# Kernel tuning notes

Hardware: AMD Instinct MI355X
Metric: run time of the kernel (lower is better)

The kernel has to match this reference:

```python
import jax, jax.numpy as jnp
import numpy as np

N, E, D, H = 50000, 800000, 128, 4
DH = D // H
BN_EPS = 1e-5


def setup_inputs() -> dict:
    key = jax.random.key(0)
    ks = jax.random.split(key, 16)
    s = 0.02
    inp = {
        "x": jax.random.normal(ks[0], (N, D), dtype=jnp.float32),
        "edge_index": jax.random.randint(ks[1], (2, E), 0, N, dtype=jnp.int64),
        "Wk": jax.random.normal(ks[2], (D, D), dtype=jnp.float32) * s,
        "bk": jnp.zeros((D,), jnp.float32),
        "Wm": jax.random.normal(ks[3], (D, D), dtype=jnp.float32) * s,
        "bm": jnp.zeros((D,), jnp.float32),
        "Wq": jax.random.normal(ks[4], (D, D), dtype=jnp.float32) * s,
        "bq": jnp.zeros((D,), jnp.float32),
        "W1": jax.random.normal(ks[5], (D, D), dtype=jnp.float32) * s,
        "b1": jnp.zeros((D,), jnp.float32),
        "gamma": jnp.ones((D,), jnp.float32),
        "beta": jnp.zeros((D,), jnp.float32),
        "W2": jax.random.normal(ks[6], (D, D), dtype=jnp.float32) * s,
        "b2": jnp.zeros((D,), jnp.float32),
    }
    return inp


def reference(x, edge_index, Wk, bk, Wm, bm, Wq, bq, W1, b1, gamma, beta, W2, b2):
    src = edge_index[0]  # [E] softmax segment key
    dst = edge_index[1]  # [E] aggregation target
    x_i = x[dst]         # [E, D] (torch code: X[1])
    x_j = x[src]         # [E, D] (torch code: X[0])

    key = (x_i @ Wk + bk).reshape(-1, H, DH)
    msg = (x_j @ Wm + bm).reshape(-1, H, DH)
    query = (x_j @ Wq + bq).reshape(-1, H, DH) / jnp.sqrt(jnp.float32(DH))

    scores = jnp.sum(query * key, axis=2)  # [E, H]

    # segment softmax over src node index (numerically stable)
    smax = jax.ops.segment_max(scores, src, num_segments=N)
    e = jnp.exp(scores - smax[src])
    ssum = jax.ops.segment_sum(e, src, num_segments=N)
    alpha = e / ssum[src]  # [E, H]

    # rescale by per-src-node edge count
    cnt = jax.ops.segment_sum(jnp.ones((scores.shape[0],), jnp.float32), src, num_segments=N)
    alpha = alpha * cnt[src][:, None]

    out_e = (msg * alpha[:, :, None]).reshape(-1, D)  # [E, D]
    out = jax.ops.segment_sum(out_e, dst, num_segments=N)  # [N, D]

    # MLP: Linear -> BatchNorm1d (training-mode batch stats) -> ReLU -> Linear
    h = out @ W1 + b1
    mean = jnp.mean(h, axis=0)
    var = jnp.var(h, axis=0)  # biased variance, as torch BN uses for normalization
    h = (h - mean) * jax.lax.rsqrt(var + BN_EPS) * gamma + beta
    h = jax.nn.relu(h)
    return h @ W2 + b2
```

## Files before the change

kernel.cpp:

```cpp
#include <hip/hip_runtime.h>
#include <hip/hip_bf16.h>

#define N_NODES 50000
#define N_EDGES 800000
#define DIM 128
#define NHEAD 4
#define GEMM_BLOCKS 782
#define HBLOCKS 313
#define EPB 2560
#define NBUCK 196
#define NBUCK2 392
#define NODE_PAD 50432
#define N2 (2 * N_NODES)

typedef __bf16 bf16x8 __attribute__((ext_vector_type(8)));
typedef __bf16 bf16x2 __attribute__((ext_vector_type(2)));
typedef float f32x4 __attribute__((ext_vector_type(4)));

struct WPtrs { const float* w[5]; };

__global__ __launch_bounds__(256) void prep_weights(WPtrs P, __bf16* __restrict__ Wt)
{
  __shared__ __bf16 tileT[16][136];
  const int mat = blockIdx.x >> 3, sl = blockIdx.x & 7;
  const float* W = P.w[mat];
  const int col0 = sl * 16;
  const int t = threadIdx.x;
  #pragma unroll
  for (int i = 0; i < 8; ++i) {
    int id = t + i * 256;
    int k = id >> 4, c = id & 15;
    tileT[c][k] = (__bf16)W[k * 128 + col0 + c];
  }
  __syncthreads();
  int c = t >> 4, kb = t & 15;
  bf16x8 v = *(const bf16x8*)&tileT[c][kb * 8];
  *(bf16x8*)&Wt[(size_t)mat * 16384 + (size_t)(col0 + c) * 128 + kb * 8] = v;
}


__device__ __forceinline__ void stage_Wt_half(const __bf16* __restrict__ Wt,
    int half, __bf16 (*wLDS)[136])
{
  const int t = threadIdx.x;
  const __bf16* base = Wt + (size_t)half * 64 * 128;
  #pragma unroll
  for (int i = 0; i < 4; ++i) {
    int id = t + i * 256;
    int col = id >> 4, kb = id & 15;
    bf16x8 v = ((const bf16x8*)(base + (size_t)col * 128))[kb];
    *(bf16x8*)&wLDS[col][kb * 8] = v;
  }
}

__device__ __forceinline__ void stage_A_f32(const float* __restrict__ A, int row0,
    int nrows, __bf16 (*aLDS)[136])
{
  const int t = threadIdx.x;
  #pragma unroll
  for (int i = 0; i < 4; ++i) {
    int id = t + i * 256;
    int r = id >> 4, cb = id & 15;
    int gr = row0 + r;
    float4 v0 = make_float4(0.f, 0.f, 0.f, 0.f), v1 = v0;
    if (gr < nrows) {
      const float4* row = (const float4*)(A + (size_t)gr * DIM);
      v0 = row[cb * 2];
      v1 = row[cb * 2 + 1];
    }
    bf16x8 o;
    o[0] = (__bf16)v0.x; o[1] = (__bf16)v0.y; o[2] = (__bf16)v0.z; o[3] = (__bf16)v0.w;
    o[4] = (__bf16)v1.x; o[5] = (__bf16)v1.y; o[6] = (__bf16)v1.z; o[7] = (__bf16)v1.w;
    *(bf16x8*)&aLDS[r][cb * 8] = o;
  }
}

__device__ __forceinline__ void stage_A_bf16(const __bf16* __restrict__ A, int row0,
    int nrows, __bf16 (*aLDS)[136])
{
  const int t = threadIdx.x;
  #pragma unroll
  for (int i = 0; i < 4; ++i) {
    int id = t + i * 256;
    int r = id >> 4, cb = id & 15;
    int gr = row0 + r;
    bf16x8 v = {};
    if (gr < nrows) v = ((const bf16x8*)(A + (size_t)gr * DIM))[cb];
    *(bf16x8*)&aLDS[r][cb * 8] = v;
  }
}

__device__ __forceinline__ void mfma_half(const __bf16 (*aLDS)[136],
    const __bf16 (*wLDS)[136], int half, f32x4 acc[8])
{
  const int lane = threadIdx.x & 63, wave = threadIdx.x >> 6;
  const int m = lane & 15, q = lane >> 4;
  #pragma unroll
  for (int kt = 0; kt < 4; ++kt) {
    bf16x8 a = *(const bf16x8*)&aLDS[wave * 16 + m][kt * 32 + q * 8];
    #pragma unroll
    for (int ct = 0; ct < 4; ++ct) {
      bf16x8 b = *(const bf16x8*)&wLDS[ct * 16 + m][kt * 32 + q * 8];
      acc[half * 4 + ct] =
          __builtin_amdgcn_mfma_f32_16x16x32_bf16(a, b, acc[half * 4 + ct], 0, 0, 0);
    }
  }
}

template <typename OutT>
__device__ __forceinline__ void store_tile(f32x4 acc[8],
    const float* __restrict__ bias, float scale, OutT* __restrict__ C,
    int row0, int nrows)
{
  const int lane = threadIdx.x & 63, wave = threadIdx.x >> 6;
  const int m = lane & 15, q = lane >> 4;
  #pragma unroll
  for (int j = 0; j < 8; ++j) {
    int col = (j >> 2) * 64 + (j & 3) * 16 + m;
    float bv = bias[col];
    #pragma unroll
    for (int r = 0; r < 4; ++r) {
      int row = row0 + wave * 16 + q * 4 + r;
      if (row < nrows) C[(size_t)row * DIM + col] = (OutT)((acc[j][r] + bv) * scale);
    }
  }
}

__device__ __forceinline__ void gemm_pass(const __bf16 (*aLDS)[136],
    __bf16 (*wLDS)[136], const __bf16* __restrict__ Wt, f32x4 acc[8])
{
  #pragma unroll
  for (int i = 0; i < 8; ++i) acc[i] = (f32x4){0.f, 0.f, 0.f, 0.f};
  stage_Wt_half(Wt, 0, wLDS);
  __syncthreads();
  mfma_half(aLDS, wLDS, 0, acc);
  __syncthreads();
  stage_Wt_half(Wt, 1, wLDS);
  __syncthreads();
  mfma_half(aLDS, wLDS, 1, acc);
}

__global__ __launch_bounds__(256) void fat1(const int* __restrict__ ei,
    int* __restrict__ hist,
    const __bf16* __restrict__ Wt, const float* __restrict__ x,
    const float* __restrict__ bk, const float* __restrict__ bm,
    const float* __restrict__ bq,
    __bf16* __restrict__ Kn, __bf16* __restrict__ Mn, __bf16* __restrict__ Qn)
{
  __shared__ __bf16 aLDS[64][136];
  __shared__ __bf16 wLDS[64][136];
  const int b = blockIdx.x, t = threadIdx.x;

  if (b < HBLOCKS) {
    int* h = (int*)&aLDS[0][0];
    for (int i = t; i < NBUCK2; i += 256) h[i] = 0;
    __syncthreads();
    #pragma unroll
    for (int i = 0; i < 10; ++i) {
      int e = b * EPB + i * 256 + t;
      if (e < N_EDGES) {
        int s = ei[e], d = ei[N_EDGES + e];
        atomicAdd(&h[s >> 8], 1);
        atomicAdd(&h[NBUCK + (d >> 8)], 1);
      }
    }
    __syncthreads();
    for (int i = t; i < NBUCK2; i += 256) hist[b * NBUCK2 + i] = h[i];
  } else {
    const int row0 = (b - HBLOCKS) * 64;
    f32x4 acc[8];
    stage_A_f32(x, row0, N_NODES, aLDS);
    gemm_pass(aLDS, wLDS, Wt, acc);
    store_tile<__bf16>(acc, bk, 1.0f, Kn, row0, N_NODES);
    __syncthreads();
    gemm_pass(aLDS, wLDS, Wt + 16384, acc);
    store_tile<__bf16>(acc, bm, 1.0f, Mn, row0, N_NODES);
    __syncthreads();
    gemm_pass(aLDS, wLDS, Wt + 32768, acc);
    store_tile<__bf16>(acc, bq, 0.17677669529663689f, Qn, row0, N_NODES);
  }
}

__global__ __launch_bounds__(64) void bucket_scan(const int* __restrict__ hist,
    int* __restrict__ bbase, int* __restrict__ tot)
{
  const int b = blockIdx.x, l = threadIdx.x;
  int run = 0;
  for (int c = 0; c < 5; ++c) {
    int idx = c * 64 + l;
    int v = (idx < HBLOCKS) ? hist[idx * NBUCK2 + b] : 0;
    int orig = v;
    #pragma unroll
    for (int o = 1; o < 64; o <<= 1) {
      int n = __shfl_up(v, o);
      if (l >= o) v += n;
    }
    if (idx < HBLOCKS) bbase[idx * NBUCK2 + b] = run + v - orig;
    run += __shfl(v, 63);
  }
  if (l == 0) tot[b] = run;
}

__global__ __launch_bounds__(256) void bucket_starts(const int* __restrict__ tot,
    int* __restrict__ bstart)
{
  __shared__ int s[256];
  const int t = threadIdx.x;
  int v = (t < NBUCK) ? tot[t] : 0;
  s[t] = v; __syncthreads();
  for (int o = 1; o < 256; o <<= 1) {
    int x = (t >= o) ? s[t - o] : 0; __syncthreads();
    s[t] += x; __syncthreads();
  }
  if (t < NBUCK) bstart[t] = s[t] - v;
  __syncthreads();
  v = (t < NBUCK) ? tot[NBUCK + t] : 0;
  s[t] = v; __syncthreads();
  for (int o = 1; o < 256; o <<= 1) {
    int x = (t >= o) ? s[t - o] : 0; __syncthreads();
    s[t] += x; __syncthreads();
  }
  if (t < NBUCK) bstart[NBUCK + t] = s[t] - v;
}

__global__ __launch_bounds__(256) void edge_scatter(const int* __restrict__ ei,
    const int* __restrict__ bbase, const int* __restrict__ bstart,
    int2* __restrict__ bucketedS, int2* __restrict__ bucketedD)
{
  __shared__ int base[NBUCK2];
  __shared__ int cur[NBUCK2];
  const int b = blockIdx.x, t = threadIdx.x;
  for (int i = t; i < NBUCK2; i += 256) {
    base[i] = bstart[i] + bbase[b * NBUCK2 + i];
    cur[i] = 0;
  }
  __syncthreads();
  #pragma unroll
  for (int i = 0; i < 10; ++i) {
    int e = b * EPB + i * 256 + t;
    if (e < N_EDGES) {
      int s = ei[e], d = ei[N_EDGES + e];
      int pk = s | (d << 16);
      int bs = s >> 8, bd = NBUCK + (d >> 8);
      int lo = atomicAdd(&cur[bs], 1);
      bucketedS[base[bs] + lo] = make_int2(pk, e);
      int ld = atomicAdd(&cur[bd], 1);
      bucketedD[base[bd] + ld] = make_int2(pk, e);
    }
  }
}

__global__ __launch_bounds__(256) void bucket_rank(const int2* __restrict__ bucketedS,
    const int2* __restrict__ bucketedD, const int* __restrict__ bstart,
    const int* __restrict__ tot,
    int2* __restrict__ elistS, int2* __restrict__ elistD,
    int* __restrict__ starts, int* __restrict__ deg,
    int* __restrict__ startsD, int* __restrict__ degD)
{
  __shared__ int c1[256], ns[256], c2[256];
  const int b = blockIdx.x, t = threadIdx.x;
  const bool srcSide = (b < NBUCK);
  const int bb = srcSide ? b : b - NBUCK;
  const int seg0 = bstart[b];
  const int cnt = tot[b];
  const int2* ent = (srcSide ? bucketedS : bucketedD) + seg0;

  c1[t] = 0; c2[t] = 0;
  __syncthreads();
  for (int i = t; i < cnt; i += 256) {
    unsigned pk = (unsigned)ent[i].x;
    int ln = (int)(srcSide ? (pk & 0xFFFFu) : (pk >> 16)) - (bb << 8);
    atomicAdd(&c1[ln], 1);
  }
  __syncthreads();
  ns[t] = c1[t]; __syncthreads();
  for (int o = 1; o < 256; o <<= 1) {
    int x = (t >= o) ? ns[t - o] : 0; __syncthreads();
    ns[t] += x; __syncthreads();
  }
  {
    int node = (bb << 8) + t;
    int nst = ns[t] - c1[t];
    if (srcSide) { starts[node] = seg0 + nst; deg[node] = c1[t]; }
    else         { startsD[node] = seg0 + nst; degD[node] = c1[t]; }
  }
  __syncthreads();
  ns[t] -= c1[t];
  __syncthreads();
  for (int i = t; i < cnt; i += 256) {
    int2 en = ent[i];
    unsigned pk = (unsigned)en.x;
    int ln = (int)(srcSide ? (pk & 0xFFFFu) : (pk >> 16)) - (bb << 8);
    int r = atomicAdd(&c2[ln], 1);
    int pos = seg0 + ns[ln] + r;
    int other = (int)(srcSide ? (pk >> 16) : (pk & 0xFFFFu));
    if (srcSide) elistS[pos] = make_int2(other, en.y);
    else         elistD[pos] = make_int2(other, en.y);
  }
}

__global__ __launch_bounds__(256) void src_scores(const int* __restrict__ starts,
    const int* __restrict__ degS, const int2* __restrict__ elistS,
    const __bf16* __restrict__ Qn, const __bf16* __restrict__ Kn,
    __bf16* __restrict__ Mn, float* __restrict__ wexp)
{
  const int wave = threadIdx.x >> 6, l = threadIdx.x & 63;
  const int n = blockIdx.x * 4 + wave;
  const int g = l >> 4, il = l & 15;
  const int h = il >> 2;
  const int beg = starts[n], end = beg + degS[n];
  if (beg == end) return;

  bf16x8 q8 = ((const bf16x8*)(Qn + (size_t)n * DIM))[il];
  float wsum = 0.f;

  for (int p0 = beg; p0 < end; p0 += 16) {
    int pp[4]; int2 en[4];
    #pragma unroll
    for (int u = 0; u < 4; ++u) {
      pp[u] = p0 + u * 4 + g;
      en[u] = elistS[min(pp[u], end - 1)];
    }
    bf16x8 kk[4];
    #pragma unroll
    for (int u = 0; u < 4; ++u)
      kk[u] = ((const bf16x8*)(Kn + (size_t)en[u].x * DIM))[il];
    #pragma unroll
    for (int u = 0; u < 4; ++u) {
      float pr = 0.f;
      #pragma unroll
      for (int j = 0; j < 8; ++j) pr += (float)q8[j] * (float)kk[u][j];
      pr += __shfl_xor(pr, 1);
      pr += __shfl_xor(pr, 2);
      float w = (pp[u] < end) ? __expf(pr) : 0.f;
      wsum += w;
      if ((pp[u] < end) && (il & 3) == 0) wexp[(size_t)en[u].y * NHEAD + h] = w;
    }
  }
  wsum += __shfl_xor(wsum, 16);
  wsum += __shfl_xor(wsum, 32);
  float factor = (float)(end - beg) / wsum;

  float fm = __shfl(factor, (l >> 4) << 2);
  bf16x2* mrow = (bf16x2*)(Mn + (size_t)n * DIM);
  bf16x2 mv = mrow[l];
  mv[0] = (__bf16)((float)mv[0] * fm);
  mv[1] = (__bf16)((float)mv[1] * fm);
  mrow[l] = mv;
}

__global__ __launch_bounds__(256) void dst_aggregate(const int* __restrict__ startsD,
    const int* __restrict__ degD, const int2* __restrict__ elistD,
    const __bf16* __restrict__ Mn, const float* __restrict__ wexp,
    __bf16* __restrict__ agg)
{
  const int wave = threadIdx.x >> 6, l = threadIdx.x & 63;
  const int n = blockIdx.x * 4 + wave;
  const int g = l >> 4, il = l & 15;
  const int h = il >> 2;
  const int beg = startsD[n], end = beg + degD[n];

  float acc[8];
  #pragma unroll
  for (int j = 0; j < 8; ++j) acc[j] = 0.f;

  for (int q0 = beg; q0 < end; q0 += 16) {
    int qq[4]; int2 ss[4];
    #pragma unroll
    for (int u = 0; u < 4; ++u) {
      qq[u] = q0 + u * 4 + g;
      ss[u] = elistD[min(qq[u], end - 1)];
    }
    float aa[4];
    #pragma unroll
    for (int u = 0; u < 4; ++u) aa[u] = wexp[(size_t)ss[u].y * NHEAD + h];
    bf16x8 mm[4];
    #pragma unroll
    for (int u = 0; u < 4; ++u)
      mm[u] = ((const bf16x8*)(Mn + (size_t)ss[u].x * DIM))[il];
    #pragma unroll
    for (int u = 0; u < 4; ++u) {
      float av = (qq[u] < end) ? aa[u] : 0.f;
      #pragma unroll
      for (int j = 0; j < 8; ++j) acc[j] += (float)mm[u][j] * av;
    }
  }
  #pragma unroll
  for (int j = 0; j < 8; ++j) {
    acc[j] += __shfl_xor(acc[j], 16);
    acc[j] += __shfl_xor(acc[j], 32);
  }
  if (g == 0) {
    bf16x8 o;
    #pragma unroll
    for (int j = 0; j < 8; ++j) o[j] = (__bf16)acc[j];
    *(bf16x8*)(agg + (size_t)n * DIM + il * 8) = o;
  }
}

__global__ __launch_bounds__(256) void gemm_stats(const __bf16* __restrict__ A,
    const __bf16* __restrict__ Wt, const float* __restrict__ bias,
    __bf16* __restrict__ C, float* __restrict__ colsum, float* __restrict__ colsq)
{
  __shared__ __bf16 aLDS[64][136];
  __shared__ __bf16 wLDS[64][136];
  __shared__ float csum[128], csq[128];
  const int t = threadIdx.x;
  const int row0 = blockIdx.x * 64;

  stage_A_bf16(A, row0, N_NODES, aLDS);
  if (t < 128) { csum[t] = 0.f; csq[t] = 0.f; }
  f32x4 acc[8];
  gemm_pass(aLDS, wLDS, Wt, acc);

  const int lane = t & 63, wave = t >> 6;
  const int m = lane & 15, q = lane >> 4;
  #pragma unroll
  for (int j = 0; j < 8; ++j) {
    int col = (j >> 2) * 64 + (j & 3) * 16 + m;
    float bv = bias[col];
    float s = 0.f, s2 = 0.f;
    #pragma unroll
    for (int r = 0; r < 4; ++r) {
      int row = row0 + wave * 16 + q * 4 + r;
      float hv = acc[j][r] + bv;
      if (row < N_NODES) {
        C[(size_t)row * DIM + col] = (__bf16)hv;
        s += hv; s2 += hv * hv;
      }
    }
    s  += __shfl_xor(s, 16);  s  += __shfl_xor(s, 32);
    s2 += __shfl_xor(s2, 16); s2 += __shfl_xor(s2, 32);
    if (q == 0) {
      atomicAdd(&csum[col], s);
      atomicAdd(&csq[col], s2);
    }
  }
  __syncthreads();
  if (t < 128) {
    atomicAdd(&colsum[t], csum[t]);
    atomicAdd(&colsq[t], csq[t]);
  }
}

__global__ __launch_bounds__(256) void gemm_bn(const __bf16* __restrict__ A,
    const __bf16* __restrict__ Wt, const float* __restrict__ bias,
    float* __restrict__ C, const float* __restrict__ colsum,
    const float* __restrict__ colsq, const float* __restrict__ gamma,
    const float* __restrict__ beta)
{
  __shared__ __bf16 aLDS[64][136];
  __shared__ __bf16 wLDS[64][136];
  __shared__ float sA[128], sB[128];
  const int t = threadIdx.x;
  const int row0 = blockIdx.x * 64;

  if (t < 128) {
    float mean = colsum[t] * (1.0f / N_NODES);
    float var = colsq[t] * (1.0f / N_NODES) - mean * mean;
    float inv = rsqrtf(var + 1e-5f);
    float a = gamma[t] * inv;
    sA[t] = a;
    sB[t] = beta[t] - mean * a;
  }
  __syncthreads();

  {
    const int cb = t & 15;
    float sa[8], sb[8];
    #pragma unroll
    for (int j = 0; j < 8; ++j) { sa[j] = sA[cb * 8 + j]; sb[j] = sB[cb * 8 + j]; }
    #pragma unroll
    for (int i = 0; i < 4; ++i) {
      int id = t + i * 256;
      int r = id >> 4;
      int gr = row0 + r;
      bf16x8 v = {};
      if (gr < N_NODES) v = ((const bf16x8*)(A + (size_t)gr * DIM))[cb];
      bf16x8 o;
      #pragma unroll
      for (int j = 0; j < 8; ++j)
        o[j] = (__bf16)fmaxf((float)v[j] * sa[j] + sb[j], 0.f);
      *(bf16x8*)&aLDS[r][cb * 8] = o;
    }
  }
  f32x4 acc[8];
  gemm_pass(aLDS, wLDS, Wt, acc);
  store_tile<float>(acc, bias, 1.0f, C, row0, N_NODES);
}

extern "C" void kernel_launch(void* const* d_in, const int* in_sizes, int n_in,
                              void* d_out, int out_size, void* d_ws, size_t ws_size,
                              hipStream_t stream) {
  const float* x     = (const float*)d_in[0];
  const int*   ei    = (const int*)d_in[1];
  const float* Wk    = (const float*)d_in[2];
  const float* bk    = (const float*)d_in[3];
  const float* Wm    = (const float*)d_in[4];
  const float* bm    = (const float*)d_in[5];
  const float* Wq    = (const float*)d_in[6];
  const float* bq    = (const float*)d_in[7];
  const float* W1    = (const float*)d_in[8];
  const float* b1    = (const float*)d_in[9];
  const float* gamma = (const float*)d_in[10];
  const float* beta  = (const float*)d_in[11];
  const float* W2    = (const float*)d_in[12];
  const float* b2    = (const float*)d_in[13];

  float* ws = (float*)d_ws;
  const size_t ND  = (size_t)N_NODES * DIM;
  const size_t NDh = ND / 2;
  const size_t EH  = (size_t)N_EDGES * NHEAD;

  __bf16* Kn   = (__bf16*)ws;
  __bf16* Mn   = (__bf16*)(ws + NDh);
  __bf16* Qn   = (__bf16*)(ws + 2 * NDh);
  __bf16* agg  = (__bf16*)(ws + 3 * NDh);
  __bf16* h1   = (__bf16*)(ws + 4 * NDh);
  float*  wexp = ws + 5 * NDh;
  int2*   bucketedS = (int2*)wexp;
  int2*   bucketedD = bucketedS + N_EDGES;
  int2*   elistS = (int2*)(wexp + EH);
  int2*   elistD = elistS + N_EDGES;
  int*    hist   = (int*)(elistD + N_EDGES);
  int*    bbase  = hist + HBLOCKS * NBUCK2;
  int*    tot    = bbase + HBLOCKS * NBUCK2;
  int*    bstart = tot + NBUCK2;
  int*    starts = bstart + NBUCK2;
  int*    deg    = starts + NODE_PAD;
  int*    startsD= deg + NODE_PAD;
  int*    degD   = startsD + NODE_PAD;
  float*  colsum = (float*)(degD + NODE_PAD);
  float*  colsq  = colsum + 128;
  __bf16* Wt     = (__bf16*)(colsq + 128);
  float*  outp   = (float*)d_out;

  hipMemsetAsync(colsum, 0, 256 * sizeof(float), stream);

  const int node_blocks = N_NODES / 4;

  WPtrs wp; wp.w[0] = Wk; wp.w[1] = Wm; wp.w[2] = Wq; wp.w[3] = W1; wp.w[4] = W2;
  prep_weights<<<40, 256, 0, stream>>>(wp, Wt);

  fat1<<<HBLOCKS + GEMM_BLOCKS, 256, 0, stream>>>(
      ei, hist, Wt, x, bk, bm, bq, Kn, Mn, Qn);

  bucket_scan<<<NBUCK2, 64, 0, stream>>>(hist, bbase, tot);
  bucket_starts<<<1, 256, 0, stream>>>(tot, bstart);
  edge_scatter<<<HBLOCKS, 256, 0, stream>>>(ei, bbase, bstart, bucketedS, bucketedD);
  bucket_rank<<<NBUCK2, 256, 0, stream>>>(bucketedS, bucketedD, bstart, tot,
                                          elistS, elistD, starts, deg,
                                          startsD, degD);

  src_scores<<<node_blocks, 256, 0, stream>>>(starts, deg, elistS, Qn, Kn, Mn, wexp);
  dst_aggregate<<<node_blocks, 256, 0, stream>>>(startsD, degD, elistD, Mn, wexp, agg);

  gemm_stats<<<GEMM_BLOCKS, 256, 0, stream>>>(agg, Wt + 3 * 16384, b1, h1,
                                              colsum, colsq);
  gemm_bn<<<GEMM_BLOCKS, 256, 0, stream>>>(h1, Wt + 4 * 16384, b2, outp,
                                           colsum, colsq, gamma, beta);
}
```

Measured before the change: 292.1 us.

## Store edge weights in dst order and stage the full weight matrix once

The bucket-rank pass is split into a dst pass, which records each edge's position in the dst-sorted list, and a src pass that carries that position. src_scores can then write edge weights directly in dst order, so dst_aggregate reads them contiguously instead of gathering by edge id. The per-src normalization factor now goes into a small per-node array instead of being applied in place to Mn, and dst_aggregate multiplies it in. The GEMMs also stage the whole 128x128 weight tile in LDS at once, replacing two halves with extra barriers, which doubles LDS use per block and may lower occupancy.

```diff
diff --git a/kernel.cpp b/kernel.cpp
--- a/kernel.cpp
+++ b/kernel.cpp
@@ -11,10 +11,8 @@
 #define NBUCK 196
 #define NBUCK2 392
 #define NODE_PAD 50432
-#define N2 (2 * N_NODES)
 
 typedef __bf16 bf16x8 __attribute__((ext_vector_type(8)));
-typedef __bf16 bf16x2 __attribute__((ext_vector_type(2)));
 typedef float f32x4 __attribute__((ext_vector_type(4)));
 
 struct WPtrs { const float* w[5]; };
@@ -39,16 +37,15 @@
 }
 
 
-__device__ __forceinline__ void stage_Wt_half(const __bf16* __restrict__ Wt,
-    int half, __bf16 (*wLDS)[136])
-{
-  const int t = threadIdx.x;
-  const __bf16* base = Wt + (size_t)half * 64 * 128;
-  #pragma unroll
-  for (int i = 0; i < 4; ++i) {
+__device__ __forceinline__ void stage_Wt_full(const __bf16* __restrict__ Wt,
+    __bf16 (*wLDS)[136])
+{
+  const int t = threadIdx.x;
+  #pragma unroll
+  for (int i = 0; i < 8; ++i) {
     int id = t + i * 256;
     int col = id >> 4, kb = id & 15;
-    bf16x8 v = ((const bf16x8*)(base + (size_t)col * 128))[kb];
+    bf16x8 v = ((const bf16x8*)(Wt + (size_t)col * 128))[kb];
     *(bf16x8*)&wLDS[col][kb * 8] = v;
   }
 }
@@ -90,21 +87,25 @@
   }
 }
 
-__device__ __forceinline__ void mfma_half(const __bf16 (*aLDS)[136],
-    const __bf16 (*wLDS)[136], int half, f32x4 acc[8])
-{
+__device__ __forceinline__ void gemm_full(const __bf16 (*aLDS)[136],
+    __bf16 (*wLDS)[136], const __bf16* __restrict__ Wt, f32x4 acc[8])
+{
+  #pragma unroll
+  for (int i = 0; i < 8; ++i) acc[i] = (f32x4){0.f, 0.f, 0.f, 0.f};
+  stage_Wt_full(Wt, wLDS);
+  __syncthreads();
   const int lane = threadIdx.x & 63, wave = threadIdx.x >> 6;
   const int m = lane & 15, q = lane >> 4;
   #pragma unroll
   for (int kt = 0; kt < 4; ++kt) {
     bf16x8 a = *(const bf16x8*)&aLDS[wave * 16 + m][kt * 32 + q * 8];
     #pragma unroll
-    for (int ct = 0; ct < 4; ++ct) {
+    for (int ct = 0; ct < 8; ++ct) {
       bf16x8 b = *(const bf16x8*)&wLDS[ct * 16 + m][kt * 32 + q * 8];
-      acc[half * 4 + ct] =
-          __builtin_amdgcn_mfma_f32_16x16x32_bf16(a, b, acc[half * 4 + ct], 0, 0, 0);
-    }
-  }
+      acc[ct] = __builtin_amdgcn_mfma_f32_16x16x32_bf16(a, b, acc[ct], 0, 0, 0);
+    }
+  }
+  __syncthreads();
 }
 
 template <typename OutT>
@@ -116,7 +117,7 @@
   const int m = lane & 15, q = lane >> 4;
   #pragma unroll
   for (int j = 0; j < 8; ++j) {
-    int col = (j >> 2) * 64 + (j & 3) * 16 + m;
+    int col = j * 16 + m;
     float bv = bias[col];
     #pragma unroll
     for (int r = 0; r < 4; ++r) {
@@ -124,20 +125,6 @@
       if (row < nrows) C[(size_t)row * DIM + col] = (OutT)((acc[j][r] + bv) * scale);
     }
   }
-}
-
-__device__ __forceinline__ void gemm_pass(const __bf16 (*aLDS)[136],
-    __bf16 (*wLDS)[136], const __bf16* __restrict__ Wt, f32x4 acc[8])
-{
-  #pragma unroll
-  for (int i = 0; i < 8; ++i) acc[i] = (f32x4){0.f, 0.f, 0.f, 0.f};
-  stage_Wt_half(Wt, 0, wLDS);
-  __syncthreads();
-  mfma_half(aLDS, wLDS, 0, acc);
-  __syncthreads();
-  stage_Wt_half(Wt, 1, wLDS);
-  __syncthreads();
-  mfma_half(aLDS, wLDS, 1, acc);
 }
 
 __global__ __launch_bounds__(256) void fat1(const int* __restrict__ ei,
@@ -148,7 +135,7 @@
     __bf16* __restrict__ Kn, __bf16* __restrict__ Mn, __bf16* __restrict__ Qn)
 {
   __shared__ __bf16 aLDS[64][136];
-  __shared__ __bf16 wLDS[64][136];
+  __shared__ __bf16 wLDS[128][136];
   const int b = blockIdx.x, t = threadIdx.x;
 
   if (b < HBLOCKS) {
@@ -170,13 +157,11 @@
     const int row0 = (b - HBLOCKS) * 64;
     f32x4 acc[8];
     stage_A_f32(x, row0, N_NODES, aLDS);
-    gemm_pass(aLDS, wLDS, Wt, acc);
+    gemm_full(aLDS, wLDS, Wt, acc);
     store_tile<__bf16>(acc, bk, 1.0f, Kn, row0, N_NODES);
-    __syncthreads();
-    gemm_pass(aLDS, wLDS, Wt + 16384, acc);
+    gemm_full(aLDS, wLDS, Wt + 16384, acc);
     store_tile<__bf16>(acc, bm, 1.0f, Mn, row0, N_NODES);
-    __syncthreads();
-    gemm_pass(aLDS, wLDS, Wt + 32768, acc);
+    gemm_full(aLDS, wLDS, Wt + 32768, acc);
     store_tile<__bf16>(acc, bq, 0.17677669529663689f, Qn, row0, N_NODES);
   }
 }
@@ -250,26 +235,23 @@
   }
 }
 
-__global__ __launch_bounds__(256) void bucket_rank(const int2* __restrict__ bucketedS,
-    const int2* __restrict__ bucketedD, const int* __restrict__ bstart,
-    const int* __restrict__ tot,
-    int2* __restrict__ elistS, int2* __restrict__ elistD,
-    int* __restrict__ starts, int* __restrict__ deg,
+__global__ __launch_bounds__(256) void bucket_rank_dst(const int2* __restrict__ bucketedD,
+    const int* __restrict__ bstart, const int* __restrict__ tot,
+    int* __restrict__ elistD, int* __restrict__ dpos,
     int* __restrict__ startsD, int* __restrict__ degD)
 {
   __shared__ int c1[256], ns[256], c2[256];
   const int b = blockIdx.x, t = threadIdx.x;
-  const bool srcSide = (b < NBUCK);
-  const int bb = srcSide ? b : b - NBUCK;
-  const int seg0 = bstart[b];
-  const int cnt = tot[b];
-  const int2* ent = (srcSide ? bucketedS : bucketedD) + seg0;
+  const int gb = NBUCK + b;
+  const int seg0 = bstart[gb];
+  const int cnt = tot[gb];
+  const int2* ent = bucketedD + seg0;
 
   c1[t] = 0; c2[t] = 0;
   __syncthreads();
   for (int i = t; i < cnt; i += 256) {
     unsigned pk = (unsigned)ent[i].x;
-    int ln = (int)(srcSide ? (pk & 0xFFFFu) : (pk >> 16)) - (bb << 8);
+    int ln = (int)(pk >> 16) - (b << 8);
     atomicAdd(&c1[ln], 1);
   }
   __syncthreads();
@@ -279,10 +261,9 @@
     ns[t] += x; __syncthreads();
   }
   {
-    int node = (bb << 8) + t;
-    int nst = ns[t] - c1[t];
-    if (srcSide) { starts[node] = seg0 + nst; deg[node] = c1[t]; }
-    else         { startsD[node] = seg0 + nst; degD[node] = c1[t]; }
+    int node = (b << 8) + t;
+    startsD[node] = seg0 + ns[t] - c1[t];
+    degD[node] = c1[t];
   }
   __syncthreads();
   ns[t] -= c1[t];
@@ -290,19 +271,60 @@
   for (int i = t; i < cnt; i += 256) {
     int2 en = ent[i];
     unsigned pk = (unsigned)en.x;
-    int ln = (int)(srcSide ? (pk & 0xFFFFu) : (pk >> 16)) - (bb << 8);
+    int ln = (int)(pk >> 16) - (b << 8);
     int r = atomicAdd(&c2[ln], 1);
     int pos = seg0 + ns[ln] + r;
-    int other = (int)(srcSide ? (pk >> 16) : (pk & 0xFFFFu));
-    if (srcSide) elistS[pos] = make_int2(other, en.y);
-    else         elistD[pos] = make_int2(other, en.y);
+    elistD[pos] = (int)(pk & 0xFFFFu);
+    dpos[en.y] = pos;
+  }
+}
+
+__global__ __launch_bounds__(256) void bucket_rank_src(const int2* __restrict__ bucketedS,
+    const int* __restrict__ bstart, const int* __restrict__ tot,
+    const int* __restrict__ dpos,
+    int2* __restrict__ elistS, int* __restrict__ starts, int* __restrict__ deg)
+{
+  __shared__ int c1[256], ns[256], c2[256];
+  const int b = blockIdx.x, t = threadIdx.x;
+  const int seg0 = bstart[b];
+  const int cnt = tot[b];
+  const int2* ent = bucketedS + seg0;
+
+  c1[t] = 0; c2[t] = 0;
+  __syncthreads();
+  for (int i = t; i < cnt; i += 256) {
+    unsigned pk = (unsigned)ent[i].x;
+    int ln = (int)(pk & 0xFFFFu) - (b << 8);
+    atomicAdd(&c1[ln], 1);
+  }
+  __syncthreads();
+  ns[t] = c1[t]; __syncthreads();
+  for (int o = 1; o < 256; o <<= 1) {
+    int x = (t >= o) ? ns[t - o] : 0; __syncthreads();
+    ns[t] += x; __syncthreads();
+  }
+  {
+    int node = (b << 8) + t;
+    starts[node] = seg0 + ns[t] - c1[t];
+    deg[node] = c1[t];
+  }
+  __syncthreads();
+  ns[t] -= c1[t];
+  __syncthreads();
+  for (int i = t; i < cnt; i += 256) {
+    int2 en = ent[i];
+    unsigned pk = (unsigned)en.x;
+    int ln = (int)(pk & 0xFFFFu) - (b << 8);
+    int r = atomicAdd(&c2[ln], 1);
+    int pos = seg0 + ns[ln] + r;
+    elistS[pos] = make_int2((int)(pk >> 16), dpos[en.y]);
   }
 }
 
 __global__ __launch_bounds__(256) void src_scores(const int* __restrict__ starts,
     const int* __restrict__ degS, const int2* __restrict__ elistS,
     const __bf16* __restrict__ Qn, const __bf16* __restrict__ Kn,
-    __bf16* __restrict__ Mn, float* __restrict__ wexp)
+    float* __restrict__ wexp, float* __restrict__ factor)
 {
   const int wave = threadIdx.x >> 6, l = threadIdx.x & 63;
   const int n = blockIdx.x * 4 + wave;
@@ -339,20 +361,14 @@
   }
   wsum += __shfl_xor(wsum, 16);
   wsum += __shfl_xor(wsum, 32);
-  float factor = (float)(end - beg) / wsum;
-
-  float fm = __shfl(factor, (l >> 4) << 2);
-  bf16x2* mrow = (bf16x2*)(Mn + (size_t)n * DIM);
-  bf16x2 mv = mrow[l];
-  mv[0] = (__bf16)((float)mv[0] * fm);
-  mv[1] = (__bf16)((float)mv[1] * fm);
-  mrow[l] = mv;
+  if (g == 0 && (il & 3) == 0)
+    factor[(size_t)n * NHEAD + h] = (float)(end - beg) / wsum;
 }
 
 __global__ __launch_bounds__(256) void dst_aggregate(const int* __restrict__ startsD,
-    const int* __restrict__ degD, const int2* __restrict__ elistD,
+    const int* __restrict__ degD, const int* __restrict__ elistD,
     const __bf16* __restrict__ Mn, const float* __restrict__ wexp,
-    __bf16* __restrict__ agg)
+    const float* __restrict__ factor, __bf16* __restrict__ agg)
 {
   const int wave = threadIdx.x >> 6, l = threadIdx.x & 63;
   const int n = blockIdx.x * 4 + wave;
@@ -365,22 +381,24 @@
   for (int j = 0; j < 8; ++j) acc[j] = 0.f;
 
   for (int q0 = beg; q0 < end; q0 += 16) {
-    int qq[4]; int2 ss[4];
+    int qq[4], ss[4]; float ww[4];
     #pragma unroll
     for (int u = 0; u < 4; ++u) {
       qq[u] = q0 + u * 4 + g;
-      ss[u] = elistD[min(qq[u], end - 1)];
-    }
-    float aa[4];
-    #pragma unroll
-    for (int u = 0; u < 4; ++u) aa[u] = wexp[(size_t)ss[u].y * NHEAD + h];
+      int cq = min(qq[u], end - 1);
+      ss[u] = elistD[cq];
+      ww[u] = wexp[(size_t)cq * NHEAD + h];
+    }
+    float ff[4];
+    #pragma unroll
+    for (int u = 0; u < 4; ++u) ff[u] = factor[(size_t)ss[u] * NHEAD + h];
     bf16x8 mm[4];
     #pragma unroll
     for (int u = 0; u < 4; ++u)
-      mm[u] = ((const bf16x8*)(Mn + (size_t)ss[u].x * DIM))[il];
+      mm[u] = ((const bf16x8*)(Mn + (size_t)ss[u] * DIM))[il];
     #pragma unroll
     for (int u = 0; u < 4; ++u) {
-      float av = (qq[u] < end) ? aa[u] : 0.f;
+      float av = (qq[u] < end) ? ww[u] * ff[u] : 0.f;
       #pragma unroll
       for (int j = 0; j < 8; ++j) acc[j] += (float)mm[u][j] * av;
     }
@@ -403,7 +421,7 @@
     __bf16* __restrict__ C, float* __restrict__ colsum, float* __restrict__ colsq)
 {
   __shared__ __bf16 aLDS[64][136];
-  __shared__ __bf16 wLDS[64][136];
+  __shared__ __bf16 wLDS[128][136];
   __shared__ float csum[128], csq[128];
   const int t = threadIdx.x;
   const int row0 = blockIdx.x * 64;
@@ -411,13 +429,13 @@
   stage_A_bf16(A, row0, N_NODES, aLDS);
   if (t < 128) { csum[t] = 0.f; csq[t] = 0.f; }
   f32x4 acc[8];
-  gemm_pass(aLDS, wLDS, Wt, acc);
+  gemm_full(aLDS, wLDS, Wt, acc);
 
   const int lane = t & 63, wave = t >> 6;
   const int m = lane & 15, q = lane >> 4;
   #pragma unroll
   for (int j = 0; j < 8; ++j) {
-    int col = (j >> 2) * 64 + (j & 3) * 16 + m;
+    int col = j * 16 + m;
     float bv = bias[col];
     float s = 0.f, s2 = 0.f;
     #pragma unroll
@@ -450,7 +468,7 @@
     const float* __restrict__ beta)
 {
   __shared__ __bf16 aLDS[64][136];
-  __shared__ __bf16 wLDS[64][136];
+  __shared__ __bf16 wLDS[128][136];
   __shared__ float sA[128], sB[128];
   const int t = threadIdx.x;
   const int row0 = blockIdx.x * 64;
@@ -485,7 +503,7 @@
     }
   }
   f32x4 acc[8];
-  gemm_pass(aLDS, wLDS, Wt, acc);
+  gemm_full(aLDS, wLDS, Wt, acc);
   store_tile<float>(acc, bias, 1.0f, C, row0, N_NODES);
 }
 
@@ -521,8 +539,9 @@
   int2*   bucketedS = (int2*)wexp;
   int2*   bucketedD = bucketedS + N_EDGES;
   int2*   elistS = (int2*)(wexp + EH);
-  int2*   elistD = elistS + N_EDGES;
-  int*    hist   = (int*)(elistD + N_EDGES);
+  int*    elistD = (int*)(elistS + N_EDGES);
+  int*    dpos   = elistD + N_EDGES;
+  int*    hist   = dpos + N_EDGES;
   int*    bbase  = hist + HBLOCKS * NBUCK2;
   int*    tot    = bbase + HBLOCKS * NBUCK2;
   int*    bstart = tot + NBUCK2;
@@ -530,7 +549,8 @@
   int*    deg    = starts + NODE_PAD;
   int*    startsD= deg + NODE_PAD;
   int*    degD   = startsD + NODE_PAD;
-  float*  colsum = (float*)(degD + NODE_PAD);
+  float*  factor = (float*)(degD + NODE_PAD);
+  float*  colsum = factor + (size_t)NHEAD * N_NODES;
   float*  colsq  = colsum + 128;
   __bf16* Wt     = (__bf16*)(colsq + 128);
   float*  outp   = (float*)d_out;
@@ -548,12 +568,15 @@
   bucket_scan<<<NBUCK2, 64, 0, stream>>>(hist, bbase, tot);
   bucket_starts<<<1, 256, 0, stream>>>(tot, bstart);
   edge_scatter<<<HBLOCKS, 256, 0, stream>>>(ei, bbase, bstart, bucketedS, bucketedD);
-  bucket_rank<<<NBUCK2, 256, 0, stream>>>(bucketedS, bucketedD, bstart, tot,
-                                          elistS, elistD, starts, deg,
-                                          startsD, degD);
-
-  src_scores<<<node_blocks, 256, 0, stream>>>(starts, deg, elistS, Qn, Kn, Mn, wexp);
-  dst_aggregate<<<node_blocks, 256, 0, stream>>>(startsD, degD, elistD, Mn, wexp, agg);
+  bucket_rank_dst<<<NBUCK, 256, 0, stream>>>(bucketedD, bstart, tot,
+                                             elistD, dpos, startsD, degD);
+  bucket_rank_src<<<NBUCK, 256, 0, stream>>>(bucketedS, bstart, tot, dpos,
+                                             elistS, starts, deg);
+
+  src_scores<<<node_blocks, 256, 0, stream>>>(starts, deg, elistS, Qn, Kn,
+                                              wexp, factor);
+  dst_aggregate<<<node_blocks, 256, 0, stream>>>(startsD, degD, elistD, Mn,
+                                                 wexp, factor, agg);
 
   gemm_stats<<<GEMM_BLOCKS, 256, 0, stream>>>(agg, Wt + 3 * 16384, b1, h1,
                                               colsum, colsq);
```

Measured after the change: 317.6 us. +8.7%, slower.

## Fuse dst aggregation into first MLP GEMM and split QKV GEMMs across blocks

Applied to the files above, without the earlier changes.

The dst-side aggregation now runs inside the W1 GEMM kernel, writing aggregated rows straight into LDS, so the agg buffer round trip and one launch go away. The softmax normalisation factor is stored per source node and head and applied during aggregation, replacing the rescale pass over Mn. Edge records are now indexed by bucket slot, so dst-side lists become 4-byte ints. The QKV projection launches three times as many blocks, one matrix each, for more parallelism at the cost of staging x three times. The fused kernel runs the gather with only 782 blocks, which may hurt latency hiding, and the 16-bit local slot index assumes dst buckets hold fewer than 65536 edges.

```diff
diff --git a/kernel.cpp b/kernel.cpp
--- a/kernel.cpp
+++ b/kernel.cpp
@@ -11,10 +11,8 @@
 #define NBUCK 196
 #define NBUCK2 392
 #define NODE_PAD 50432
-#define N2 (2 * N_NODES)
 
 typedef __bf16 bf16x8 __attribute__((ext_vector_type(8)));
-typedef __bf16 bf16x2 __attribute__((ext_vector_type(2)));
 typedef float f32x4 __attribute__((ext_vector_type(4)));
 
 struct WPtrs { const float* w[5]; };
@@ -167,17 +165,16 @@
     __syncthreads();
     for (int i = t; i < NBUCK2; i += 256) hist[b * NBUCK2 + i] = h[i];
   } else {
-    const int row0 = (b - HBLOCKS) * 64;
+    const int gb = b - HBLOCKS;
+    const int mat = gb % 3;
+    const int row0 = (gb / 3) * 64;
+    const float* bias = (mat == 0) ? bk : (mat == 1) ? bm : bq;
+    __bf16* out = (mat == 0) ? Kn : (mat == 1) ? Mn : Qn;
+    const float scale = (mat == 2) ? 0.17677669529663689f : 1.0f;
     f32x4 acc[8];
     stage_A_f32(x, row0, N_NODES, aLDS);
-    gemm_pass(aLDS, wLDS, Wt, acc);
-    store_tile<__bf16>(acc, bk, 1.0f, Kn, row0, N_NODES);
-    __syncthreads();
-    gemm_pass(aLDS, wLDS, Wt + 16384, acc);
-    store_tile<__bf16>(acc, bm, 1.0f, Mn, row0, N_NODES);
-    __syncthreads();
-    gemm_pass(aLDS, wLDS, Wt + 32768, acc);
-    store_tile<__bf16>(acc, bq, 0.17677669529663689f, Qn, row0, N_NODES);
+    gemm_pass(aLDS, wLDS, Wt + (size_t)mat * 16384, acc);
+    store_tile<__bf16>(acc, bias, scale, out, row0, N_NODES);
   }
 }
 
@@ -225,7 +222,7 @@
 
 __global__ __launch_bounds__(256) void edge_scatter(const int* __restrict__ ei,
     const int* __restrict__ bbase, const int* __restrict__ bstart,
-    int2* __restrict__ bucketedS, int2* __restrict__ bucketedD)
+    int2* __restrict__ bucketedS, int* __restrict__ bucketedD)
 {
   __shared__ int base[NBUCK2];
   __shared__ int cur[NBUCK2];
@@ -243,17 +240,18 @@
       int pk = s | (d << 16);
       int bs = s >> 8, bd = NBUCK + (d >> 8);
       int lo = atomicAdd(&cur[bs], 1);
-      bucketedS[base[bs] + lo] = make_int2(pk, e);
       int ld = atomicAdd(&cur[bd], 1);
-      bucketedD[base[bd] + ld] = make_int2(pk, e);
+      int slotD = base[bd] + ld;
+      bucketedS[base[bs] + lo] = make_int2(pk, slotD);
+      bucketedD[slotD] = pk;
     }
   }
 }
 
 __global__ __launch_bounds__(256) void bucket_rank(const int2* __restrict__ bucketedS,
-    const int2* __restrict__ bucketedD, const int* __restrict__ bstart,
+    const int* __restrict__ bucketedD, const int* __restrict__ bstart,
     const int* __restrict__ tot,
-    int2* __restrict__ elistS, int2* __restrict__ elistD,
+    int2* __restrict__ elistS, int* __restrict__ elistD,
     int* __restrict__ starts, int* __restrict__ deg,
     int* __restrict__ startsD, int* __restrict__ degD)
 {
@@ -263,14 +261,17 @@
   const int bb = srcSide ? b : b - NBUCK;
   const int seg0 = bstart[b];
   const int cnt = tot[b];
-  const int2* ent = (srcSide ? bucketedS : bucketedD) + seg0;
 
   c1[t] = 0; c2[t] = 0;
   __syncthreads();
-  for (int i = t; i < cnt; i += 256) {
-    unsigned pk = (unsigned)ent[i].x;
-    int ln = (int)(srcSide ? (pk & 0xFFFFu) : (pk >> 16)) - (bb << 8);
-    atomicAdd(&c1[ln], 1);
+  if (srcSide) {
+    const int2* ent = bucketedS + seg0;
+    for (int i = t; i < cnt; i += 256)
+      atomicAdd(&c1[(int)((unsigned)ent[i].x & 0xFFFFu) - (bb << 8)], 1);
+  } else {
+    const int* ent = bucketedD + seg0;
+    for (int i = t; i < cnt; i += 256)
+      atomicAdd(&c1[(int)((unsigned)ent[i] >> 16) - (bb << 8)], 1);
   }
   __syncthreads();
   ns[t] = c1[t]; __syncthreads();
@@ -280,29 +281,37 @@
   }
   {
     int node = (bb << 8) + t;
-    int nst = ns[t] - c1[t];
-    if (srcSide) { starts[node] = seg0 + nst; deg[node] = c1[t]; }
-    else         { startsD[node] = seg0 + nst; degD[node] = c1[t]; }
+    int st = seg0 + ns[t] - c1[t];
+    if (srcSide) { starts[node] = st; deg[node] = c1[t]; }
+    else         { startsD[node] = st; degD[node] = c1[t]; }
   }
   __syncthreads();
   ns[t] -= c1[t];
   __syncthreads();
-  for (int i = t; i < cnt; i += 256) {
-    int2 en = ent[i];
-    unsigned pk = (unsigned)en.x;
-    int ln = (int)(srcSide ? (pk & 0xFFFFu) : (pk >> 16)) - (bb << 8);
-    int r = atomicAdd(&c2[ln], 1);
-    int pos = seg0 + ns[ln] + r;
-    int other = (int)(srcSide ? (pk >> 16) : (pk & 0xFFFFu));
-    if (srcSide) elistS[pos] = make_int2(other, en.y);
-    else         elistD[pos] = make_int2(other, en.y);
+  if (srcSide) {
+    const int2* ent = bucketedS + seg0;
+    for (int i = t; i < cnt; i += 256) {
+      int2 en = ent[i];
+      unsigned pk = (unsigned)en.x;
+      int ln = (int)(pk & 0xFFFFu) - (bb << 8);
+      int r = atomicAdd(&c2[ln], 1);
+      elistS[seg0 + ns[ln] + r] = make_int2((int)(pk >> 16), en.y);
+    }
+  } else {
+    const int* ent = bucketedD + seg0;
+    for (int i = t; i < cnt; i += 256) {
+      unsigned pk = (unsigned)ent[i];
+      int ln = (int)(pk >> 16) - (bb << 8);
+      int r = atomicAdd(&c2[ln], 1);
+      elistD[seg0 + ns[ln] + r] = (int)(pk & 0xFFFFu) | (i << 16);
+    }
   }
 }
 
 __global__ __launch_bounds__(256) void src_scores(const int* __restrict__ starts,
     const int* __restrict__ degS, const int2* __restrict__ elistS,
     const __bf16* __restrict__ Qn, const __bf16* __restrict__ Kn,
-    __bf16* __restrict__ Mn, float* __restrict__ wexp)
+    float* __restrict__ wexp, float* __restrict__ factor)
 {
   const int wave = threadIdx.x >> 6, l = threadIdx.x & 63;
   const int n = blockIdx.x * 4 + wave;
@@ -339,66 +348,15 @@
   }
   wsum += __shfl_xor(wsum, 16);
   wsum += __shfl_xor(wsum, 32);
-  float factor = (float)(end - beg) / wsum;
-
-  float fm = __shfl(factor, (l >> 4) << 2);
-  bf16x2* mrow = (bf16x2*)(Mn + (size_t)n * DIM);
-  bf16x2 mv = mrow[l];
-  mv[0] = (__bf16)((float)mv[0] * fm);
-  mv[1] = (__bf16)((float)mv[1] * fm);
-  mrow[l] = mv;
-}
-
-__global__ __launch_bounds__(256) void dst_aggregate(const int* __restrict__ startsD,
-    const int* __restrict__ degD, const int2* __restrict__ elistD,
+  if (g == 0 && (il & 3) == 0)
+    factor[(size_t)n * NHEAD + h] = (float)(end - beg) / wsum;
+}
+
+__global__ __launch_bounds__(256) void agg_gemm_stats(const int* __restrict__ startsD,
+    const int* __restrict__ degD, const int* __restrict__ elistD,
+    const int* __restrict__ bstart,
     const __bf16* __restrict__ Mn, const float* __restrict__ wexp,
-    __bf16* __restrict__ agg)
-{
-  const int wave = threadIdx.x >> 6, l = threadIdx.x & 63;
-  const int n = blockIdx.x * 4 + wave;
-  const int g = l >> 4, il = l & 15;
-  const int h = il >> 2;
-  const int beg = startsD[n], end = beg + degD[n];
-
-  float acc[8];
-  #pragma unroll
-  for (int j = 0; j < 8; ++j) acc[j] = 0.f;
-
-  for (int q0 = beg; q0 < end; q0 += 16) {
-    int qq[4]; int2 ss[4];
-    #pragma unroll
-    for (int u = 0; u < 4; ++u) {
-      qq[u] = q0 + u * 4 + g;
-      ss[u] = elistD[min(qq[u], end - 1)];
-    }
-    float aa[4];
-    #pragma unroll
-    for (int u = 0; u < 4; ++u) aa[u] = wexp[(size_t)ss[u].y * NHEAD + h];
-    bf16x8 mm[4];
-    #pragma unroll
-    for (int u = 0; u < 4; ++u)
-      mm[u] = ((const bf16x8*)(Mn + (size_t)ss[u].x * DIM))[il];
-    #pragma unroll
-    for (int u = 0; u < 4; ++u) {
-      float av = (qq[u] < end) ? aa[u] : 0.f;
-      #pragma unroll
-      for (int j = 0; j < 8; ++j) acc[j] += (float)mm[u][j] * av;
-    }
-  }
-  #pragma unroll
-  for (int j = 0; j < 8; ++j) {
-    acc[j] += __shfl_xor(acc[j], 16);
-    acc[j] += __shfl_xor(acc[j], 32);
-  }
-  if (g == 0) {
-    bf16x8 o;
-    #pragma unroll
-    for (int j = 0; j < 8; ++j) o[j] = (__bf16)acc[j];
-    *(bf16x8*)(agg + (size_t)n * DIM + il * 8) = o;
-  }
-}
-
-__global__ __launch_bounds__(256) void gemm_stats(const __bf16* __restrict__ A,
+    const float* __restrict__ factor,
     const __bf16* __restrict__ Wt, const float* __restrict__ bias,
     __bf16* __restrict__ C, float* __restrict__ colsum, float* __restrict__ colsq)
 {
@@ -407,14 +365,60 @@
   __shared__ float csum[128], csq[128];
   const int t = threadIdx.x;
   const int row0 = blockIdx.x * 64;
-
-  stage_A_bf16(A, row0, N_NODES, aLDS);
+  const int wave = t >> 6, l = t & 63;
+  const int g = l >> 4, il = l & 15;
+  const int h = il >> 2;
+  const int seg0d = bstart[NBUCK + (row0 >> 8)];
+
   if (t < 128) { csum[t] = 0.f; csq[t] = 0.f; }
+
+  for (int k = 0; k < 16; ++k) {
+    const int n = row0 + wave * 16 + k;
+    const int beg = startsD[n], end = beg + degD[n];
+    float acc[8];
+    #pragma unroll
+    for (int j = 0; j < 8; ++j) acc[j] = 0.f;
+
+    for (int q0 = beg; q0 < end; q0 += 16) {
+      int qq[4], ss[4]; float ww[4];
+      #pragma unroll
+      for (int u = 0; u < 4; ++u) {
+        qq[u] = q0 + u * 4 + g;
+        int cq = min(qq[u], end - 1);
+        int v = elistD[cq];
+        ss[u] = v & 0xFFFF;
+        ww[u] = wexp[(size_t)(seg0d + ((unsigned)v >> 16)) * NHEAD + h];
+      }
+      float ff[4];
+      #pragma unroll
+      for (int u = 0; u < 4; ++u) ff[u] = factor[(size_t)ss[u] * NHEAD + h];
+      bf16x8 mm[4];
+      #pragma unroll
+      for (int u = 0; u < 4; ++u)
+        mm[u] = ((const bf16x8*)(Mn + (size_t)ss[u] * DIM))[il];
+      #pragma unroll
+      for (int u = 0; u < 4; ++u) {
+        float av = (qq[u] < end) ? ww[u] * ff[u] : 0.f;
+        #pragma unroll
+        for (int j = 0; j < 8; ++j) acc[j] += (float)mm[u][j] * av;
+      }
+    }
+    #pragma unroll
+    for (int j = 0; j < 8; ++j) {
+      acc[j] += __shfl_xor(acc[j], 16);
+      acc[j] += __shfl_xor(acc[j], 32);
+    }
+    if (g == 0) {
+      bf16x8 o;
+      #pragma unroll
+      for (int j = 0; j < 8; ++j) o[j] = (__bf16)acc[j];
+      *(bf16x8*)&aLDS[wave * 16 + k][il * 8] = o;
+    }
+  }
   f32x4 acc[8];
   gemm_pass(aLDS, wLDS, Wt, acc);
 
-  const int lane = t & 63, wave = t >> 6;
-  const int m = lane & 15, q = lane >> 4;
+  const int m = l & 15, q = l >> 4;
   #pragma unroll
   for (int j = 0; j < 8; ++j) {
     int col = (j >> 2) * 64 + (j & 3) * 16 + m;
@@ -515,14 +519,13 @@
   __bf16* Kn   = (__bf16*)ws;
   __bf16* Mn   = (__bf16*)(ws + NDh);
   __bf16* Qn   = (__bf16*)(ws + 2 * NDh);
-  __bf16* agg  = (__bf16*)(ws + 3 * NDh);
-  __bf16* h1   = (__bf16*)(ws + 4 * NDh);
-  float*  wexp = ws + 5 * NDh;
+  __bf16* h1   = (__bf16*)(ws + 3 * NDh);
+  float*  wexp = ws + 4 * NDh;
   int2*   bucketedS = (int2*)wexp;
-  int2*   bucketedD = bucketedS + N_EDGES;
+  int*    bucketedD = (int*)(bucketedS + N_EDGES);
   int2*   elistS = (int2*)(wexp + EH);
-  int2*   elistD = elistS + N_EDGES;
-  int*    hist   = (int*)(elistD + N_EDGES);
+  int*    elistD = (int*)(elistS + N_EDGES);
+  int*    hist   = elistD + N_EDGES;
   int*    bbase  = hist + HBLOCKS * NBUCK2;
   int*    tot    = bbase + HBLOCKS * NBUCK2;
   int*    bstart = tot + NBUCK2;
@@ -530,7 +533,8 @@
   int*    deg    = starts + NODE_PAD;
   int*    startsD= deg + NODE_PAD;
   int*    degD   = startsD + NODE_PAD;
-  float*  colsum = (float*)(degD + NODE_PAD);
+  float*  factor = (float*)(degD + NODE_PAD);
+  float*  colsum = factor + (size_t)NHEAD * N_NODES;
   float*  colsq  = colsum + 128;
   __bf16* Wt     = (__bf16*)(colsq + 128);
   float*  outp   = (float*)d_out;
@@ -542,7 +546,7 @@
   WPtrs wp; wp.w[0] = Wk; wp.w[1] = Wm; wp.w[2] = Wq; wp.w[3] = W1; wp.w[4] = W2;
   prep_weights<<<40, 256, 0, stream>>>(wp, Wt);
 
-  fat1<<<HBLOCKS + GEMM_BLOCKS, 256, 0, stream>>>(
+  fat1<<<HBLOCKS + 3 * GEMM_BLOCKS, 256, 0, stream>>>(
       ei, hist, Wt, x, bk, bm, bq, Kn, Mn, Qn);
 
   bucket_scan<<<NBUCK2, 64, 0, stream>>>(hist, bbase, tot);
@@ -552,11 +556,13 @@
                                           elistS, elistD, starts, deg,
                                           startsD, degD);
 
-  src_scores<<<node_blocks, 256, 0, stream>>>(starts, deg, elistS, Qn, Kn, Mn, wexp);
-  dst_aggregate<<<node_blocks, 256, 0, stream>>>(startsD, degD, elistD, Mn, wexp, agg);
-
-  gemm_stats<<<GEMM_BLOCKS, 256, 0, stream>>>(agg, Wt + 3 * 16384, b1, h1,
-                                              colsum, colsq);
+  src_scores<<<node_blocks, 256, 0, stream>>>(starts, deg, elistS, Qn, Kn,
+                                              wexp, factor);
+
+  agg_gemm_stats<<<GEMM_BLOCKS, 256, 0, stream>>>(startsD, degD, elistD, bstart,
+                                                  Mn, wexp, factor,
+                                                  Wt + 3 * 16384, b1, h1,
+                                                  colsum, colsq);
   gemm_bn<<<GEMM_BLOCKS, 256, 0, stream>>>(h1, Wt + 4 * 16384, b2, outp,
                                            colsum, colsq, gamma, beta);
 }
```

Result: no change. 291.5 us (-0.2%).
